# Kernel optimization log

Hardware: AMD Instinct MI355X
Metric: run time of the kernel (lower is better)

## Reference

```python
import jax, jax.numpy as jnp
import numpy as np

MARGIN = 0.5
EPS = 1e-5


def setup_inputs() -> dict:
    key = jax.random.key(0)
    k1, k2 = jax.random.split(key)
    n, d, n_new, n_old = 8192, 256, 4096, 4096
    feature = jax.random.normal(k1, (n, d), dtype=jnp.float32)
    target = jax.random.randint(k2, (n,), 0, 100, dtype=jnp.int64)
    new_idx = jnp.arange(n_new, dtype=jnp.int64)
    old_idx = jnp.arange(n_old, dtype=jnp.int64)
    return {"feature": feature, "target": target, "new_idx": new_idx, "old_idx": old_idx}


def _triplet_loss(feature, target, new_idx, old_idx):
    n = feature.shape[0]
    n_new = new_idx.shape[0]
    # alpha switch is based on static shape, exactly as in the torch code
    alpha = 0.9 if old_idx.shape[0] != 0 else 0.5

    sim = feature @ feature.T                      # [n, n]
    sim_new = sim[:, new_idx]                      # [n, n_new]
    t_new = target[new_idx]                        # [n_new]

    same_new = target[:, None] == t_new[None, :]   # [n, n_new]
    is_new_row = jnp.arange(n) < n_new             # [n]

    # positive pairs (only defined for rows i < n_new)
    pos_mask = same_new & (sim_new < 1.0 - EPS)
    pos_loss_new = jnp.sum(jnp.where(pos_mask, 1.0 - sim_new, 0.0), axis=1)  # [n]
    # faithful to the torch bug: rows i >= n_new reuse the stale pos_pair_
    # from the last new row (i = n_new - 1)
    stale_pos = pos_loss_new[n_new - 1]
    pos_loss = jnp.where(is_new_row, pos_loss_new, stale_pos)

    # negatives: new rows scan all columns, old rows scan only new_idx columns
    diff_all = target[:, None] != target[None, :]
    neg_all = jnp.sum(jnp.where(diff_all & (sim > MARGIN), sim, 0.0), axis=1)
    neg_newcols = jnp.sum(jnp.where((~same_new) & (sim_new > MARGIN), sim_new, 0.0), axis=1)
    neg_loss = jnp.where(is_new_row, neg_all, neg_newcols)

    return jnp.mean(alpha * pos_loss + (1.0 - alpha) * neg_loss)


def reference(feature, target, new_idx, old_idx):
    return _triplet_loss(feature, target, new_idx, old_idx)
```

## Files before the change

### kernel.cpp

```cpp
#include <hip/hip_runtime.h>
#include <hip/hip_bf16.h>
#include <stdint.h>

#define MARGIN   0.5f
#define POS_THR  (1.0f - 1e-5f)

typedef __attribute__((ext_vector_type(8))) short  short8;
typedef __attribute__((ext_vector_type(4))) float  f32x4;

#define BM 128
#define BN 128
#define BK 32
#define NPANEL_SHIFT 7
#define NSLOTS 256
#define MAXN_HIST 8192

__device__ __forceinline__ ushort f2bf_rne(float x) {
  uint32_t u = __float_as_uint(x);
  u += 0x7fffu + ((u >> 16) & 1u);
  return (ushort)(u >> 16);
}

__device__ __forceinline__ void async_load16(const ushort* g, ushort* l) {
  __builtin_amdgcn_global_load_lds(
      (__attribute__((address_space(1))) void*)(const_cast<ushort*>(g)),
      (__attribute__((address_space(3))) void*)(l),
      16, 0, 0);
}

__global__ void prep_kernel(const float* __restrict__ src, ushort* __restrict__ dst,
                            const int* __restrict__ new_idx,
                            int* __restrict__ cnt, int* __restrict__ flags,
                            float* __restrict__ misc,
                            int total8, int n, int npanel, int n_new, int convBlocks) {
  __shared__ int hcnt[MAXN_HIST];
  __shared__ int hflag[MAXN_HIST / BN];
  const int tid = threadIdx.x;
  if ((int)blockIdx.x < convBlocks) {
    int i = blockIdx.x * blockDim.x + tid;
    if (i < total8) {
      const float4* s4 = reinterpret_cast<const float4*>(src);
      float4 a = s4[i * 2], b = s4[i * 2 + 1];
      short8 o;
      o[0] = (short)f2bf_rne(a.x); o[1] = (short)f2bf_rne(a.y);
      o[2] = (short)f2bf_rne(a.z); o[3] = (short)f2bf_rne(a.w);
      o[4] = (short)f2bf_rne(b.x); o[5] = (short)f2bf_rne(b.y);
      o[6] = (short)f2bf_rne(b.z); o[7] = (short)f2bf_rne(b.w);
      reinterpret_cast<short8*>(dst)[i] = o;
    }
    return;
  }
  for (int i = tid; i < n; i += blockDim.x) hcnt[i] = 0;
  for (int i = tid; i < npanel; i += blockDim.x) hflag[i] = 0;
  __syncthreads();
  for (int i = tid; i < n_new; i += blockDim.x) atomicAdd(&hcnt[new_idx[i]], 1);
  __syncthreads();
  for (int i = tid; i < n; i += blockDim.x) {
    int c = hcnt[i];
    cnt[i] = c;
    if (c) atomicOr(&hflag[i >> NPANEL_SHIFT], 1);
  }
  __syncthreads();
  for (int i = tid; i < npanel; i += blockDim.x) flags[i] = hflag[i];
  for (int i = tid; i < NSLOTS + 1; i += blockDim.x) misc[i] = 0.f;
}

__global__ __launch_bounds__(256) void simloss_kernel(
    const ushort* __restrict__ fb, const int* __restrict__ target,
    const int* __restrict__ cnt, const int* __restrict__ flags,
    float* __restrict__ misc, int d, int n_new, float alpha) {
  __shared__ __align__(16) ushort Als[3][BM * BK];
  __shared__ __align__(16) ushort Bls[3][BN * BK];
  __shared__ int   t_row[BM];
  __shared__ int   t_col[BN];
  __shared__ float cw_col[BN];
  __shared__ float cw_row[BM];
  __shared__ float red[4];

  const int bx = blockIdx.x, by = blockIdx.y;
  if (bx > by) return;
  const int tid = threadIdx.x;
  const int rowBase = by * BM;
  const int colBase = bx * BN;
  const bool diag = (bx == by);

  if ((rowBase >= n_new && flags[bx] == 0) &&
      (colBase >= n_new && flags[by] == 0)) return;

  if (tid < BM) {
    t_row[tid]  = target[rowBase + tid];
    cw_row[tid] = (float)cnt[rowBase + tid];
  }
  if (tid < BN) {
    t_col[tid]  = target[colBase + tid];
    cw_col[tid] = (float)cnt[colBase + tid];
  }

  const int lane = tid & 63;
  const int wid  = tid >> 6;
  const int wr   = wid >> 1;
  const int wc   = wid & 1;
  const int l15  = lane & 15;
  const int kb   = lane >> 4;

  const int ch0 = (wid * 2 + 0) * 64 + lane;
  const int ch1 = (wid * 2 + 1) * 64 + lane;
  const int r0 = ch0 >> 2, kq0 = (ch0 & 3) ^ ((ch0 >> 3) & 3);
  const int r1 = ch1 >> 2, kq1 = (ch1 & 3) ^ ((ch1 >> 3) & 3);
  const ushort* gA0 = fb + (size_t)(rowBase + r0) * d + kq0 * 8;
  const ushort* gA1 = fb + (size_t)(rowBase + r1) * d + kq1 * 8;
  const ushort* gB0 = fb + (size_t)(colBase + r0) * d + kq0 * 8;
  const ushort* gB1 = fb + (size_t)(colBase + r1) * d + kq1 * 8;
  const int lo0 = (wid * 2 + 0) * 512;
  const int lo1 = (wid * 2 + 1) * 512;

  f32x4 acc[4][4] = {};

  int aoff[4], boff[4];
#pragma unroll
  for (int m = 0; m < 4; ++m) {
    int row = wr * 64 + m * 16 + l15;
    aoff[m] = row * 32 + ((kb ^ ((row >> 1) & 3)) * 8);
  }
#pragma unroll
  for (int nf = 0; nf < 4; ++nf) {
    int row = wc * 64 + nf * 16 + l15;
    boff[nf] = row * 32 + ((kb ^ ((row >> 1) & 3)) * 8);
  }

  asm volatile("s_waitcnt vmcnt(0) lgkmcnt(0)" ::: "memory");
  __builtin_amdgcn_sched_barrier(0);

  async_load16(gA0, &Als[0][lo0]);
  async_load16(gA1, &Als[0][lo1]);
  async_load16(gB0, &Bls[0][lo0]);
  async_load16(gB1, &Bls[0][lo1]);
  const int nk = d / BK;
  if (nk > 1) {
    async_load16(gA0 + BK, &Als[1][lo0]);
    async_load16(gA1 + BK, &Als[1][lo1]);
    async_load16(gB0 + BK, &Bls[1][lo0]);
    async_load16(gB1 + BK, &Bls[1][lo1]);
  }

  int cur = 0;
  for (int t = 0; t < nk; ++t) {
    if (t == nk - 1) asm volatile("s_waitcnt vmcnt(0)" ::: "memory");
    else             asm volatile("s_waitcnt vmcnt(4)" ::: "memory");
    __builtin_amdgcn_s_barrier();
    __builtin_amdgcn_sched_barrier(0);

    if (t + 2 < nk) {
      int nxt = cur + 2; if (nxt >= 3) nxt -= 3;
      int ko = (t + 2) * BK;
      async_load16(gA0 + ko, &Als[nxt][lo0]);
      async_load16(gA1 + ko, &Als[nxt][lo1]);
      async_load16(gB0 + ko, &Bls[nxt][lo0]);
      async_load16(gB1 + ko, &Bls[nxt][lo1]);
    }

    short8 afr[4], bfr[4];
#pragma unroll
    for (int m = 0; m < 4; ++m)
      afr[m] = *reinterpret_cast<const short8*>(&Als[cur][aoff[m]]);
#pragma unroll
    for (int nf = 0; nf < 4; ++nf)
      bfr[nf] = *reinterpret_cast<const short8*>(&Bls[cur][boff[nf]]);
    asm volatile("s_waitcnt lgkmcnt(0)" ::: "memory");
    __builtin_amdgcn_sched_barrier(0);

#pragma unroll
    for (int m = 0; m < 4; ++m)
#pragma unroll
      for (int nf = 0; nf < 4; ++nf)
        acc[m][nf] = __builtin_amdgcn_mfma_f32_16x16x32_bf16(bfr[nf], afr[m], acc[m][nf], 0, 0, 0);

    cur = (cur + 1 == 3) ? 0 : cur + 1;
  }

  const float beta = 1.0f - alpha;
  int tc_r[4][4]; float cw_c[4][4]; bool cn_r[4][4];
#pragma unroll
  for (int nf = 0; nf < 4; ++nf)
#pragma unroll
    for (int q = 0; q < 4; ++q) {
      int cl = wc * 64 + nf * 16 + kb * 4 + q;
      tc_r[nf][q] = t_col[cl];
      cw_c[nf][q] = cw_col[cl];
      cn_r[nf][q] = (colBase + cl) < n_new;
    }

  const int  stale_row = n_new - 1;
  const bool blk_stale = (stale_row >= rowBase) && (stale_row < rowBase + BM);
  const int  srl = stale_row - rowBase;

  float tot = 0.f;
#pragma unroll
  for (int m = 0; m < 4; ++m) {
    int rl = wr * 64 + m * 16 + l15;
    int r  = rowBase + rl;
    int tr = t_row[rl];
    bool rnew = (r < n_new);
    float cwr  = cw_row[rl];
    float acwr = alpha * cwr;
    float bcwr = beta * cwr;
    float p = 0.f, ng = 0.f, t2 = 0.f;
#pragma unroll
    for (int nf = 0; nf < 4; ++nf)
#pragma unroll
      for (int q = 0; q < 4; ++q) {
        float s = acc[m][nf][q];
        bool same = (tr == tc_r[nf][q]);
        bool gm = (s > MARGIN);
        bool lp = (s < POS_THR);
        if (rnew) {
          if (same && lp) p  += cw_c[nf][q] * (1.0f - s);
          if (!same && gm) ng += s;
        } else {
          if (!same && gm) ng += cw_c[nf][q] * s;
        }
        if (cn_r[nf][q]) {
          if (same && lp)  t2 += acwr * (1.0f - s);
          if (!same && gm) t2 += beta * s;
        } else {
          if (!same && gm) t2 += bcwr * s;
        }
      }
    if (blk_stale && wr == (srl >> 6) && m == ((srl >> 4) & 3)) {
      float pr = p;
      pr += __shfl_xor(pr, 16); pr += __shfl_xor(pr, 32);
      if (lane < 16 && rl == srl) atomicAdd(&misc[NSLOTS], pr);
    }
    tot += rnew ? fmaf(alpha, p, beta * ng) : beta * ng;
    if (!diag) tot += t2;
  }
#pragma unroll
  for (int off = 32; off; off >>= 1) tot += __shfl_xor(tot, off);
  if (lane == 0) red[wid] = tot;
  __syncthreads();
  if (tid == 0)
    atomicAdd(&misc[(by * gridDim.x + bx) & (NSLOTS - 1)],
              red[0] + red[1] + red[2] + red[3]);
}

__global__ void finalize_kernel(const float* __restrict__ misc,
                                float* __restrict__ out, int n, int n_new,
                                float alpha) {
  int t = threadIdx.x;
  float c = misc[t] + misc[t + 64] + misc[t + 128] + misc[t + 192];
#pragma unroll
  for (int off = 32; off; off >>= 1) c += __shfl_xor(c, off);
  if (t == 0)
    out[0] = (c + (float)(n - n_new) * alpha * misc[NSLOTS]) / (float)n;
}

extern "C" void kernel_launch(void* const* d_in, const int* in_sizes, int n_in,
                              void* d_out, int out_size, void* d_ws, size_t ws_size,
                              hipStream_t stream) {
  const float* feature = (const float*)d_in[0];
  const int*   target  = (const int*)d_in[1];
  const int*   new_idx = (const int*)d_in[2];

  const int n     = in_sizes[1];
  const int d     = in_sizes[0] / n;
  const int n_new = in_sizes[2];
  const int n_old = (n_in > 3) ? in_sizes[3] : 0;
  const float alpha = (n_old != 0) ? 0.9f : 0.5f;
  const int npanel = n / BN;

  auto al = [](size_t x) { return (x + 255) & ~(size_t)255; };
  char* ws = (char*)d_ws;
  ushort* fb    = (ushort*)ws;
  size_t  off   = al((size_t)n * d * sizeof(ushort));
  int*    cnt   = (int*)(ws + off);   off += al((size_t)n * sizeof(int));
  int*    flags = (int*)(ws + off);   off += al((size_t)npanel * sizeof(int));
  float*  misc  = (float*)(ws + off);

  int total8 = (n * d) / 8;
  int convBlocks = (total8 + 255) / 256;
  prep_kernel<<<convBlocks + 1, 256, 0, stream>>>(feature, fb, new_idx, cnt, flags,
                                                  misc, total8, n, npanel,
                                                  n_new, convBlocks);

  dim3 grid(n / BN, n / BM);
  simloss_kernel<<<grid, 256, 0, stream>>>(fb, target, cnt, flags, misc,
                                           d, n_new, alpha);

  finalize_kernel<<<1, 64, 0, stream>>>(misc, (float*)d_out, n, n_new, alpha);
}
```

Before: 125.8 us.

## Use persistent blocks over a compacted tile list with cross-tile prefetch

The prep kernel now builds a compacted list of active lower-triangle tiles with a prefix scan, and packs target and count into one int2 metadata array. The similarity kernel becomes persistent: 512 blocks walk the list and prefetch the next tile's first K stages and metadata while the current tile finishes, using a 4-stage buffer. This removes launch and early-exit cost for the many skipped blocks and hides pipeline fill latency between tiles. It also adds a serial list build inside one prep block and fixed hand-tuned vmcnt counts that depend on d/BK being 8.

```diff
diff --git a/kernel.cpp b/kernel.cpp
--- a/kernel.cpp
+++ b/kernel.cpp
@@ -11,9 +11,9 @@
 #define BM 128
 #define BN 128
 #define BK 32
-#define NPANEL_SHIFT 7
 #define NSLOTS 256
 #define MAXN_HIST 8192
+#define NB 512
 
 __device__ __forceinline__ ushort f2bf_rne(float x) {
   uint32_t u = __float_as_uint(x);
@@ -28,13 +28,14 @@
       16, 0, 0);
 }
 
-__global__ void prep_kernel(const float* __restrict__ src, ushort* __restrict__ dst,
-                            const int* __restrict__ new_idx,
-                            int* __restrict__ cnt, int* __restrict__ flags,
-                            float* __restrict__ misc,
-                            int total8, int n, int npanel, int n_new, int convBlocks) {
-  __shared__ int hcnt[MAXN_HIST];
-  __shared__ int hflag[MAXN_HIST / BN];
+#define WAITV(N) asm volatile("s_waitcnt vmcnt(" #N ")" ::: "memory")
+
+__global__ __launch_bounds__(256) void prep_kernel(
+    const float* __restrict__ src, ushort* __restrict__ dst,
+    const int* __restrict__ target, const int* __restrict__ new_idx,
+    int2* __restrict__ metaG, int* __restrict__ list, int* __restrict__ nActG,
+    float* __restrict__ misc, int total8, int n, int npanel, int n_new,
+    int convBlocks) {
   const int tid = threadIdx.x;
   if ((int)blockIdx.x < convBlocks) {
     int i = blockIdx.x * blockDim.x + tid;
@@ -50,71 +51,88 @@
     }
     return;
   }
-  for (int i = tid; i < n; i += blockDim.x) hcnt[i] = 0;
-  for (int i = tid; i < npanel; i += blockDim.x) hflag[i] = 0;
-  __syncthreads();
-  for (int i = tid; i < n_new; i += blockDim.x) atomicAdd(&hcnt[new_idx[i]], 1);
-  __syncthreads();
-  for (int i = tid; i < n; i += blockDim.x) {
+  __shared__ int hcnt[MAXN_HIST];
+  __shared__ int hflag[MAXN_HIST / BN];
+  __shared__ int pcnt[256];
+  for (int i = tid; i < n; i += 256) hcnt[i] = 0;
+  for (int i = tid; i < npanel; i += 256) hflag[i] = 0;
+  __syncthreads();
+  for (int i = tid; i < n_new; i += 256) atomicAdd(&hcnt[new_idx[i]], 1);
+  __syncthreads();
+  for (int i = tid; i < n; i += 256) {
     int c = hcnt[i];
-    cnt[i] = c;
-    if (c) atomicOr(&hflag[i >> NPANEL_SHIFT], 1);
-  }
-  __syncthreads();
-  for (int i = tid; i < npanel; i += blockDim.x) flags[i] = hflag[i];
-  for (int i = tid; i < NSLOTS + 1; i += blockDim.x) misc[i] = 0.f;
-}
-
-__global__ __launch_bounds__(256) void simloss_kernel(
-    const ushort* __restrict__ fb, const int* __restrict__ target,
-    const int* __restrict__ cnt, const int* __restrict__ flags,
+    metaG[i] = make_int2(target[i], __float_as_int((float)c));
+    if (c) atomicOr(&hflag[i >> 7], 1);
+  }
+  for (int i = tid; i < NSLOTS + 1; i += 256) misc[i] = 0.f;
+  __syncthreads();
+  const int P  = npanel;
+  const int TP = P * (P + 1) / 2;
+  const int C  = (TP + 255) / 256;
+  int l0 = tid * C, l1 = min(l0 + C, TP);
+  int cnt_t = 0;
+  int by = 0, bx = 0;
+  if (l0 < TP) {
+    by = (int)((sqrtf(8.f * (float)l0 + 1.f) - 1.f) * 0.5f);
+    while ((by + 1) * (by + 2) / 2 <= l0) by++;
+    while (by * (by + 1) / 2 > l0) by--;
+    bx = l0 - by * (by + 1) / 2;
+    int tby = by, tbx = bx;
+    for (int l = l0; l < l1; ++l) {
+      bool rowOld = tby * BM >= n_new, colOld = tbx * BN >= n_new;
+      if (!((rowOld && hflag[tbx] == 0) && (colOld && hflag[tby] == 0))) cnt_t++;
+      if (++tbx > tby) { tby++; tbx = 0; }
+    }
+  }
+  pcnt[tid] = cnt_t;
+  __syncthreads();
+  for (int off = 1; off < 256; off <<= 1) {
+    int v = (tid >= off) ? pcnt[tid - off] : 0;
+    __syncthreads();
+    pcnt[tid] += v;
+    __syncthreads();
+  }
+  int pos = pcnt[tid] - cnt_t;
+  if (tid == 255) *nActG = pcnt[255];
+  if (l0 < TP) {
+    for (int l = l0; l < l1; ++l) {
+      bool rowOld = by * BM >= n_new, colOld = bx * BN >= n_new;
+      if (!((rowOld && hflag[bx] == 0) && (colOld && hflag[by] == 0)))
+        list[pos++] = (by << 16) | bx;
+      if (++bx > by) { by++; bx = 0; }
+    }
+  }
+}
+
+__global__ __launch_bounds__(256, 2) void simloss_kernel(
+    const ushort* __restrict__ fb, const int2* __restrict__ metaG,
+    const int* __restrict__ list, const int* __restrict__ nActG,
     float* __restrict__ misc, int d, int n_new, float alpha) {
-  __shared__ __align__(16) ushort Als[3][BM * BK];
-  __shared__ __align__(16) ushort Bls[3][BN * BK];
-  __shared__ int   t_row[BM];
-  __shared__ int   t_col[BN];
-  __shared__ float cw_col[BN];
-  __shared__ float cw_row[BM];
+  __shared__ __align__(16) ushort Als[4][BM * BK];
+  __shared__ __align__(16) ushort Bls[4][BN * BK];
+  __shared__ __align__(16) int2  metaRl[2][BM];
+  __shared__ __align__(16) int2  metaCl[2][BN];
   __shared__ float red[4];
 
-  const int bx = blockIdx.x, by = blockIdx.y;
-  if (bx > by) return;
-  const int tid = threadIdx.x;
-  const int rowBase = by * BM;
-  const int colBase = bx * BN;
-  const bool diag = (bx == by);
-
-  if ((rowBase >= n_new && flags[bx] == 0) &&
-      (colBase >= n_new && flags[by] == 0)) return;
-
-  if (tid < BM) {
-    t_row[tid]  = target[rowBase + tid];
-    cw_row[tid] = (float)cnt[rowBase + tid];
-  }
-  if (tid < BN) {
-    t_col[tid]  = target[colBase + tid];
-    cw_col[tid] = (float)cnt[colBase + tid];
-  }
-
+  const int bid  = blockIdx.x;
+  const int nAct = *nActG;
+  if (bid >= nAct) return;
+
+  const int tid  = threadIdx.x;
   const int lane = tid & 63;
   const int wid  = tid >> 6;
   const int wr   = wid >> 1;
   const int wc   = wid & 1;
   const int l15  = lane & 15;
   const int kb   = lane >> 4;
+  const float beta = 1.0f - alpha;
 
   const int ch0 = (wid * 2 + 0) * 64 + lane;
   const int ch1 = (wid * 2 + 1) * 64 + lane;
   const int r0 = ch0 >> 2, kq0 = (ch0 & 3) ^ ((ch0 >> 3) & 3);
   const int r1 = ch1 >> 2, kq1 = (ch1 & 3) ^ ((ch1 >> 3) & 3);
-  const ushort* gA0 = fb + (size_t)(rowBase + r0) * d + kq0 * 8;
-  const ushort* gA1 = fb + (size_t)(rowBase + r1) * d + kq1 * 8;
-  const ushort* gB0 = fb + (size_t)(colBase + r0) * d + kq0 * 8;
-  const ushort* gB1 = fb + (size_t)(colBase + r1) * d + kq1 * 8;
   const int lo0 = (wid * 2 + 0) * 512;
   const int lo1 = (wid * 2 + 1) * 512;
-
-  f32x4 acc[4][4] = {};
 
   int aoff[4], boff[4];
 #pragma unroll
@@ -128,119 +146,156 @@
     boff[nf] = row * 32 + ((kb ^ ((row >> 1) & 3)) * 8);
   }
 
+  int w  = bid;
+  int pk = list[w];
+  int curRow = (pk >> 16) * BM, curCol = (pk & 0xffff) * BN;
+  const ushort* cA0 = fb + (size_t)(curRow + r0) * d + kq0 * 8;
+  const ushort* cA1 = fb + (size_t)(curRow + r1) * d + kq1 * 8;
+  const ushort* cB0 = fb + (size_t)(curCol + r0) * d + kq0 * 8;
+  const ushort* cB1 = fb + (size_t)(curCol + r1) * d + kq1 * 8;
+  const ushort* cMR = (const ushort*)(metaG + curRow) + (size_t)lane * 8;
+  const ushort* cMC = (const ushort*)(metaG + curCol) + (size_t)lane * 8;
+
+  f32x4 acc[4][4] = {};
+  float tot = 0.f;
+  int mp = 0;
+
   asm volatile("s_waitcnt vmcnt(0) lgkmcnt(0)" ::: "memory");
   __builtin_amdgcn_sched_barrier(0);
-
-  async_load16(gA0, &Als[0][lo0]);
-  async_load16(gA1, &Als[0][lo1]);
-  async_load16(gB0, &Bls[0][lo0]);
-  async_load16(gB1, &Bls[0][lo1]);
-  const int nk = d / BK;
-  if (nk > 1) {
-    async_load16(gA0 + BK, &Als[1][lo0]);
-    async_load16(gA1 + BK, &Als[1][lo1]);
-    async_load16(gB0 + BK, &Bls[1][lo0]);
-    async_load16(gB1 + BK, &Bls[1][lo1]);
-  }
-
-  int cur = 0;
-  for (int t = 0; t < nk; ++t) {
-    if (t == nk - 1) asm volatile("s_waitcnt vmcnt(0)" ::: "memory");
-    else             asm volatile("s_waitcnt vmcnt(4)" ::: "memory");
-    __builtin_amdgcn_s_barrier();
-    __builtin_amdgcn_sched_barrier(0);
-
-    if (t + 2 < nk) {
-      int nxt = cur + 2; if (nxt >= 3) nxt -= 3;
-      int ko = (t + 2) * BK;
-      async_load16(gA0 + ko, &Als[nxt][lo0]);
-      async_load16(gA1 + ko, &Als[nxt][lo1]);
-      async_load16(gB0 + ko, &Bls[nxt][lo0]);
-      async_load16(gB1 + ko, &Bls[nxt][lo1]);
-    }
-
-    short8 afr[4], bfr[4];
-#pragma unroll
-    for (int m = 0; m < 4; ++m)
-      afr[m] = *reinterpret_cast<const short8*>(&Als[cur][aoff[m]]);
-#pragma unroll
-    for (int nf = 0; nf < 4; ++nf)
-      bfr[nf] = *reinterpret_cast<const short8*>(&Bls[cur][boff[nf]]);
-    asm volatile("s_waitcnt lgkmcnt(0)" ::: "memory");
-    __builtin_amdgcn_sched_barrier(0);
-
-#pragma unroll
-    for (int m = 0; m < 4; ++m)
-#pragma unroll
-      for (int nf = 0; nf < 4; ++nf)
-        acc[m][nf] = __builtin_amdgcn_mfma_f32_16x16x32_bf16(bfr[nf], afr[m], acc[m][nf], 0, 0, 0);
-
-    cur = (cur + 1 == 3) ? 0 : cur + 1;
-  }
-
-  const float beta = 1.0f - alpha;
-  int tc_r[4][4]; float cw_c[4][4]; bool cn_r[4][4];
-#pragma unroll
-  for (int nf = 0; nf < 4; ++nf)
-#pragma unroll
-    for (int q = 0; q < 4; ++q) {
-      int cl = wc * 64 + nf * 16 + kb * 4 + q;
-      tc_r[nf][q] = t_col[cl];
-      cw_c[nf][q] = cw_col[cl];
-      cn_r[nf][q] = (colBase + cl) < n_new;
-    }
-
-  const int  stale_row = n_new - 1;
-  const bool blk_stale = (stale_row >= rowBase) && (stale_row < rowBase + BM);
-  const int  srl = stale_row - rowBase;
-
-  float tot = 0.f;
-#pragma unroll
-  for (int m = 0; m < 4; ++m) {
-    int rl = wr * 64 + m * 16 + l15;
-    int r  = rowBase + rl;
-    int tr = t_row[rl];
-    bool rnew = (r < n_new);
-    float cwr  = cw_row[rl];
-    float acwr = alpha * cwr;
-    float bcwr = beta * cwr;
-    float p = 0.f, ng = 0.f, t2 = 0.f;
-#pragma unroll
-    for (int nf = 0; nf < 4; ++nf)
-#pragma unroll
-      for (int q = 0; q < 4; ++q) {
-        float s = acc[m][nf][q];
-        bool same = (tr == tc_r[nf][q]);
-        bool gm = (s > MARGIN);
-        bool lp = (s < POS_THR);
-        if (rnew) {
-          if (same && lp) p  += cw_c[nf][q] * (1.0f - s);
-          if (!same && gm) ng += s;
+#define STAGE4(pa0, pa1, pb0, pb1, p)                                          \
+  { async_load16((pa0) + (p) * BK, &Als[(p) & 3][lo0]);                        \
+    async_load16((pa1) + (p) * BK, &Als[(p) & 3][lo1]);                        \
+    async_load16((pb0) + (p) * BK, &Bls[(p) & 3][lo0]);                        \
+    async_load16((pb1) + (p) * BK, &Bls[(p) & 3][lo1]); }
+  STAGE4(cA0, cA1, cB0, cB1, 0);
+  async_load16(cMR, (ushort*)&metaRl[0][0]);
+  async_load16(cMC, (ushort*)&metaCl[0][0]);
+  STAGE4(cA0, cA1, cB0, cB1, 1);
+  STAGE4(cA0, cA1, cB0, cB1, 2);
+
+  for (;;) {
+    const bool hasNext = (w + NB) < nAct;
+    const int  pkN = hasNext ? list[w + NB] : pk;
+    const int  nxtRow = (pkN >> 16) * BM, nxtCol = (pkN & 0xffff) * BN;
+    const ushort* nA0 = fb + (size_t)(nxtRow + r0) * d + kq0 * 8;
+    const ushort* nA1 = fb + (size_t)(nxtRow + r1) * d + kq1 * 8;
+    const ushort* nB0 = fb + (size_t)(nxtCol + r0) * d + kq0 * 8;
+    const ushort* nB1 = fb + (size_t)(nxtCol + r1) * d + kq1 * 8;
+    const ushort* nMR = (const ushort*)(metaG + nxtRow) + (size_t)lane * 8;
+    const ushort* nMC = (const ushort*)(metaG + nxtCol) + (size_t)lane * 8;
+
+#pragma unroll
+    for (int i = 0; i < 8; ++i) {
+      if (i < 6)        WAITV(8);
+      else if (i == 6)  { if (hasNext) WAITV(10); else WAITV(4); }
+      else              { if (hasNext) WAITV(10); else WAITV(0); }
+      __builtin_amdgcn_s_barrier();
+      __builtin_amdgcn_sched_barrier(0);
+
+      if (i <= 4) {
+        STAGE4(cA0, cA1, cB0, cB1, i + 3);
+      } else if (hasNext) {
+        if (i == 5) {
+          STAGE4(nA0, nA1, nB0, nB1, 0);
+          async_load16(nMR, (ushort*)&metaRl[mp ^ 1][0]);
+          async_load16(nMC, (ushort*)&metaCl[mp ^ 1][0]);
+        } else if (i == 6) {
+          STAGE4(nA0, nA1, nB0, nB1, 1);
         } else {
-          if (!same && gm) ng += cw_c[nf][q] * s;
-        }
-        if (cn_r[nf][q]) {
-          if (same && lp)  t2 += acwr * (1.0f - s);
-          if (!same && gm) t2 += beta * s;
-        } else {
-          if (!same && gm) t2 += bcwr * s;
+          STAGE4(nA0, nA1, nB0, nB1, 2);
         }
       }
-    if (blk_stale && wr == (srl >> 6) && m == ((srl >> 4) & 3)) {
-      float pr = p;
-      pr += __shfl_xor(pr, 16); pr += __shfl_xor(pr, 32);
-      if (lane < 16 && rl == srl) atomicAdd(&misc[NSLOTS], pr);
-    }
-    tot += rnew ? fmaf(alpha, p, beta * ng) : beta * ng;
-    if (!diag) tot += t2;
-  }
+
+      short8 afr[4], bfr[4];
+      const ushort* As = &Als[i & 3][0];
+      const ushort* Bs = &Bls[i & 3][0];
+#pragma unroll
+      for (int m = 0; m < 4; ++m)
+        afr[m] = *reinterpret_cast<const short8*>(&As[aoff[m]]);
+#pragma unroll
+      for (int nf = 0; nf < 4; ++nf)
+        bfr[nf] = *reinterpret_cast<const short8*>(&Bs[boff[nf]]);
+      asm volatile("s_waitcnt lgkmcnt(0)" ::: "memory");
+      __builtin_amdgcn_sched_barrier(0);
+
+#pragma unroll
+      for (int m = 0; m < 4; ++m)
+#pragma unroll
+        for (int nf = 0; nf < 4; ++nf)
+          acc[m][nf] = __builtin_amdgcn_mfma_f32_16x16x32_bf16(bfr[nf], afr[m], acc[m][nf], 0, 0, 0);
+    }
+
+    {
+      const bool diag = (curRow == curCol);
+      int tcr[4][4]; float cwc[4][4]; bool cnr[4][4];
+#pragma unroll
+      for (int nf = 0; nf < 4; ++nf)
+#pragma unroll
+        for (int q = 0; q < 4; ++q) {
+          int cl = wc * 64 + nf * 16 + kb * 4 + q;
+          int2 mc = metaCl[mp][cl];
+          tcr[nf][q] = mc.x;
+          cwc[nf][q] = __int_as_float(mc.y);
+          cnr[nf][q] = (curCol + cl) < n_new;
+        }
+      const int  stale_row = n_new - 1;
+      const bool blk_stale = (stale_row >= curRow) && (stale_row < curRow + BM);
+      const int  srl = stale_row - curRow;
+#pragma unroll
+      for (int m = 0; m < 4; ++m) {
+        int rl = wr * 64 + m * 16 + l15;
+        int r  = curRow + rl;
+        int2 mr = metaRl[mp][rl];
+        int   tr  = mr.x;
+        float cwr = __int_as_float(mr.y);
+        bool rnew = (r < n_new);
+        float acwr = alpha * cwr, bcwr = beta * cwr;
+        float p = 0.f, ng = 0.f, t2 = 0.f;
+#pragma unroll
+        for (int nf = 0; nf < 4; ++nf)
+#pragma unroll
+          for (int q = 0; q < 4; ++q) {
+            float s = acc[m][nf][q];
+            bool same = (tr == tcr[nf][q]);
+            bool gm = (s > MARGIN);
+            bool lp = (s < POS_THR);
+            if (rnew) {
+              if (same && lp)  p  += cwc[nf][q] * (1.0f - s);
+              if (!same && gm) ng += s;
+            } else {
+              if (!same && gm) ng += cwc[nf][q] * s;
+            }
+            if (cnr[nf][q]) {
+              if (same && lp)  t2 += acwr * (1.0f - s);
+              if (!same && gm) t2 += beta * s;
+            } else {
+              if (!same && gm) t2 += bcwr * s;
+            }
+          }
+        if (blk_stale && wr == (srl >> 6) && m == ((srl >> 4) & 3)) {
+          float pr = p;
+          pr += __shfl_xor(pr, 16); pr += __shfl_xor(pr, 32);
+          if (lane < 16 && rl == srl) atomicAdd(&misc[NSLOTS], pr);
+        }
+        tot += rnew ? fmaf(alpha, p, beta * ng) : beta * ng;
+        if (!diag) tot += t2;
+        acc[m][0] = f32x4{}; acc[m][1] = f32x4{};
+        acc[m][2] = f32x4{}; acc[m][3] = f32x4{};
+      }
+    }
+
+    if (!hasNext) break;
+    w += NB; pk = pkN; mp ^= 1;
+    curRow = nxtRow; curCol = nxtCol;
+    cA0 = nA0; cA1 = nA1; cB0 = nB0; cB1 = nB1;
+  }
+
 #pragma unroll
   for (int off = 32; off; off >>= 1) tot += __shfl_xor(tot, off);
   if (lane == 0) red[wid] = tot;
   __syncthreads();
   if (tid == 0)
-    atomicAdd(&misc[(by * gridDim.x + bx) & (NSLOTS - 1)],
-              red[0] + red[1] + red[2] + red[3]);
+    atomicAdd(&misc[bid & (NSLOTS - 1)], red[0] + red[1] + red[2] + red[3]);
 }
 
 __global__ void finalize_kernel(const float* __restrict__ misc,
@@ -267,24 +322,26 @@
   const int n_old = (n_in > 3) ? in_sizes[3] : 0;
   const float alpha = (n_old != 0) ? 0.9f : 0.5f;
   const int npanel = n / BN;
+  const int maxTiles = npanel * (npanel + 1) / 2;
 
   auto al = [](size_t x) { return (x + 255) & ~(size_t)255; };
   char* ws = (char*)d_ws;
   ushort* fb    = (ushort*)ws;
   size_t  off   = al((size_t)n * d * sizeof(ushort));
-  int*    cnt   = (int*)(ws + off);   off += al((size_t)n * sizeof(int));
-  int*    flags = (int*)(ws + off);   off += al((size_t)npanel * sizeof(int));
+  int2*   metaG = (int2*)(ws + off);  off += al((size_t)n * sizeof(int2));
+  int*    list  = (int*)(ws + off);   off += al((size_t)maxTiles * sizeof(int));
+  int*    nAct  = (int*)(ws + off);   off += al(sizeof(int));
   float*  misc  = (float*)(ws + off);
 
   int total8 = (n * d) / 8;
   int convBlocks = (total8 + 255) / 256;
-  prep_kernel<<<convBlocks + 1, 256, 0, stream>>>(feature, fb, new_idx, cnt, flags,
-                                                  misc, total8, n, npanel,
-                                                  n_new, convBlocks);
-
-  dim3 grid(n / BN, n / BM);
-  simloss_kernel<<<grid, 256, 0, stream>>>(fb, target, cnt, flags, misc,
-                                           d, n_new, alpha);
+  prep_kernel<<<convBlocks + 1, 256, 0, stream>>>(feature, fb, target, new_idx,
+                                                  metaG, list, nAct, misc,
+                                                  total8, n, npanel, n_new,
+                                                  convBlocks);
+
+  simloss_kernel<<<NB, 256, 0, stream>>>(fb, metaG, list, nAct, misc,
+                                         d, n_new, alpha);
 
   finalize_kernel<<<1, 64, 0, stream>>>(misc, (float*)d_out, n, n_new, alpha);
 }
```

After: 123.4 us. No clear change (-1.9%).

## Load MFMA fragments directly from global memory and launch only lower-triangle tiles

Applied to the files above, without the earlier changes.

Drops the LDS triple-buffered async-load pipeline and has each wave read its bf16 MFMA fragments straight from global memory, relying on L2/L1 reuse. It launches a 1D grid over only the lower-triangular tiles, recovering (bx,by) with a sqrt-based index decode, instead of a square grid where half the blocks exit at once. It also packs target and count into one int2 metadata array built in the prep kernel, so each tile needs fewer metadata loads. The risk is that uncoalesced per-lane 16-byte global loads, with no staging through shared memory, cost more than the LDS pipeline and the removed early-exit blocks saved.

```diff
diff --git a/kernel.cpp b/kernel.cpp
--- a/kernel.cpp
+++ b/kernel.cpp
@@ -10,8 +10,6 @@
 
 #define BM 128
 #define BN 128
-#define BK 32
-#define NPANEL_SHIFT 7
 #define NSLOTS 256
 #define MAXN_HIST 8192
 
@@ -21,20 +19,11 @@
   return (ushort)(u >> 16);
 }
 
-__device__ __forceinline__ void async_load16(const ushort* g, ushort* l) {
-  __builtin_amdgcn_global_load_lds(
-      (__attribute__((address_space(1))) void*)(const_cast<ushort*>(g)),
-      (__attribute__((address_space(3))) void*)(l),
-      16, 0, 0);
-}
-
-__global__ void prep_kernel(const float* __restrict__ src, ushort* __restrict__ dst,
-                            const int* __restrict__ new_idx,
-                            int* __restrict__ cnt, int* __restrict__ flags,
-                            float* __restrict__ misc,
-                            int total8, int n, int npanel, int n_new, int convBlocks) {
-  __shared__ int hcnt[MAXN_HIST];
-  __shared__ int hflag[MAXN_HIST / BN];
+__global__ __launch_bounds__(256) void prep_kernel(
+    const float* __restrict__ src, ushort* __restrict__ dst,
+    const int* __restrict__ target, const int* __restrict__ new_idx,
+    int2* __restrict__ metaG, int* __restrict__ flags, float* __restrict__ misc,
+    int total8, int n, int npanel, int n_new, int convBlocks) {
   const int tid = threadIdx.x;
   if ((int)blockIdx.x < convBlocks) {
     int i = blockIdx.x * blockDim.x + tid;
@@ -50,52 +39,43 @@
     }
     return;
   }
-  for (int i = tid; i < n; i += blockDim.x) hcnt[i] = 0;
-  for (int i = tid; i < npanel; i += blockDim.x) hflag[i] = 0;
-  __syncthreads();
-  for (int i = tid; i < n_new; i += blockDim.x) atomicAdd(&hcnt[new_idx[i]], 1);
-  __syncthreads();
-  for (int i = tid; i < n; i += blockDim.x) {
+  __shared__ int hcnt[MAXN_HIST];
+  __shared__ int hflag[MAXN_HIST / BN];
+  for (int i = tid; i < n; i += 256) hcnt[i] = 0;
+  for (int i = tid; i < npanel; i += 256) hflag[i] = 0;
+  __syncthreads();
+  for (int i = tid; i < n_new; i += 256) atomicAdd(&hcnt[new_idx[i]], 1);
+  __syncthreads();
+  for (int i = tid; i < n; i += 256) {
     int c = hcnt[i];
-    cnt[i] = c;
-    if (c) atomicOr(&hflag[i >> NPANEL_SHIFT], 1);
-  }
-  __syncthreads();
-  for (int i = tid; i < npanel; i += blockDim.x) flags[i] = hflag[i];
-  for (int i = tid; i < NSLOTS + 1; i += blockDim.x) misc[i] = 0.f;
+    metaG[i] = make_int2(target[i], __float_as_int((float)c));
+    if (c) atomicOr(&hflag[i >> 7], 1);
+  }
+  __syncthreads();
+  for (int i = tid; i < npanel; i += 256) flags[i] = hflag[i];
+  for (int i = tid; i < NSLOTS + 1; i += 256) misc[i] = 0.f;
 }
 
 __global__ __launch_bounds__(256) void simloss_kernel(
-    const ushort* __restrict__ fb, const int* __restrict__ target,
-    const int* __restrict__ cnt, const int* __restrict__ flags,
-    float* __restrict__ misc, int d, int n_new, float alpha) {
-  __shared__ __align__(16) ushort Als[3][BM * BK];
-  __shared__ __align__(16) ushort Bls[3][BN * BK];
-  __shared__ int   t_row[BM];
-  __shared__ int   t_col[BN];
-  __shared__ float cw_col[BN];
-  __shared__ float cw_row[BM];
+    const ushort* __restrict__ fb, const int2* __restrict__ metaG,
+    const int* __restrict__ flags, float* __restrict__ misc,
+    int d, int n_new, float alpha) {
+  __shared__ int2 metaR[BM];
+  __shared__ int2 metaC[BN];
   __shared__ float red[4];
 
-  const int bx = blockIdx.x, by = blockIdx.y;
-  if (bx > by) return;
-  const int tid = threadIdx.x;
+  const int l = blockIdx.x;
+  int by = (int)((sqrtf(8.f * (float)l + 1.f) - 1.f) * 0.5f);
+  while ((by + 1) * (by + 2) / 2 <= l) by++;
+  while (by * (by + 1) / 2 > l) by--;
+  const int bx = l - by * (by + 1) / 2;
+
   const int rowBase = by * BM;
   const int colBase = bx * BN;
-  const bool diag = (bx == by);
-
   if ((rowBase >= n_new && flags[bx] == 0) &&
       (colBase >= n_new && flags[by] == 0)) return;
 
-  if (tid < BM) {
-    t_row[tid]  = target[rowBase + tid];
-    cw_row[tid] = (float)cnt[rowBase + tid];
-  }
-  if (tid < BN) {
-    t_col[tid]  = target[colBase + tid];
-    cw_col[tid] = (float)cnt[colBase + tid];
-  }
-
+  const int tid  = threadIdx.x;
   const int lane = tid & 63;
   const int wid  = tid >> 6;
   const int wr   = wid >> 1;
@@ -103,91 +83,43 @@
   const int l15  = lane & 15;
   const int kb   = lane >> 4;
 
-  const int ch0 = (wid * 2 + 0) * 64 + lane;
-  const int ch1 = (wid * 2 + 1) * 64 + lane;
-  const int r0 = ch0 >> 2, kq0 = (ch0 & 3) ^ ((ch0 >> 3) & 3);
-  const int r1 = ch1 >> 2, kq1 = (ch1 & 3) ^ ((ch1 >> 3) & 3);
-  const ushort* gA0 = fb + (size_t)(rowBase + r0) * d + kq0 * 8;
-  const ushort* gA1 = fb + (size_t)(rowBase + r1) * d + kq1 * 8;
-  const ushort* gB0 = fb + (size_t)(colBase + r0) * d + kq0 * 8;
-  const ushort* gB1 = fb + (size_t)(colBase + r1) * d + kq1 * 8;
-  const int lo0 = (wid * 2 + 0) * 512;
-  const int lo1 = (wid * 2 + 1) * 512;
+  if (tid < BM)        metaR[tid]       = metaG[rowBase + tid];
+  else if (tid < 256)  metaC[tid - 128] = metaG[colBase + (tid - 128)];
+  __syncthreads();
+
+  const ushort* pA = fb + (size_t)(rowBase + wr * 64 + l15) * d + kb * 8;
+  const ushort* pB = fb + (size_t)(colBase + wc * 64 + l15) * d + kb * 8;
 
   f32x4 acc[4][4] = {};
-
-  int aoff[4], boff[4];
-#pragma unroll
-  for (int m = 0; m < 4; ++m) {
-    int row = wr * 64 + m * 16 + l15;
-    aoff[m] = row * 32 + ((kb ^ ((row >> 1) & 3)) * 8);
-  }
-#pragma unroll
-  for (int nf = 0; nf < 4; ++nf) {
-    int row = wc * 64 + nf * 16 + l15;
-    boff[nf] = row * 32 + ((kb ^ ((row >> 1) & 3)) * 8);
-  }
-
-  asm volatile("s_waitcnt vmcnt(0) lgkmcnt(0)" ::: "memory");
-  __builtin_amdgcn_sched_barrier(0);
-
-  async_load16(gA0, &Als[0][lo0]);
-  async_load16(gA1, &Als[0][lo1]);
-  async_load16(gB0, &Bls[0][lo0]);
-  async_load16(gB1, &Bls[0][lo1]);
-  const int nk = d / BK;
-  if (nk > 1) {
-    async_load16(gA0 + BK, &Als[1][lo0]);
-    async_load16(gA1 + BK, &Als[1][lo1]);
-    async_load16(gB0 + BK, &Bls[1][lo0]);
-    async_load16(gB1 + BK, &Bls[1][lo1]);
-  }
-
-  int cur = 0;
-  for (int t = 0; t < nk; ++t) {
-    if (t == nk - 1) asm volatile("s_waitcnt vmcnt(0)" ::: "memory");
-    else             asm volatile("s_waitcnt vmcnt(4)" ::: "memory");
-    __builtin_amdgcn_s_barrier();
-    __builtin_amdgcn_sched_barrier(0);
-
-    if (t + 2 < nk) {
-      int nxt = cur + 2; if (nxt >= 3) nxt -= 3;
-      int ko = (t + 2) * BK;
-      async_load16(gA0 + ko, &Als[nxt][lo0]);
-      async_load16(gA1 + ko, &Als[nxt][lo1]);
-      async_load16(gB0 + ko, &Bls[nxt][lo0]);
-      async_load16(gB1 + ko, &Bls[nxt][lo1]);
-    }
-
+  const int nk = d >> 5;
+#pragma unroll 2
+  for (int ks = 0; ks < nk; ++ks) {
     short8 afr[4], bfr[4];
 #pragma unroll
     for (int m = 0; m < 4; ++m)
-      afr[m] = *reinterpret_cast<const short8*>(&Als[cur][aoff[m]]);
+      afr[m] = *reinterpret_cast<const short8*>(pA + (size_t)m * 16 * d + ks * 32);
 #pragma unroll
     for (int nf = 0; nf < 4; ++nf)
-      bfr[nf] = *reinterpret_cast<const short8*>(&Bls[cur][boff[nf]]);
-    asm volatile("s_waitcnt lgkmcnt(0)" ::: "memory");
-    __builtin_amdgcn_sched_barrier(0);
-
+      bfr[nf] = *reinterpret_cast<const short8*>(pB + (size_t)nf * 16 * d + ks * 32);
 #pragma unroll
     for (int m = 0; m < 4; ++m)
 #pragma unroll
       for (int nf = 0; nf < 4; ++nf)
         acc[m][nf] = __builtin_amdgcn_mfma_f32_16x16x32_bf16(bfr[nf], afr[m], acc[m][nf], 0, 0, 0);
-
-    cur = (cur + 1 == 3) ? 0 : cur + 1;
   }
 
   const float beta = 1.0f - alpha;
-  int tc_r[4][4]; float cw_c[4][4]; bool cn_r[4][4];
+  const bool diag = (bx == by);
+  int tcr[4][4]; float cwc[4][4]; bool cnr[4][4];
 #pragma unroll
   for (int nf = 0; nf < 4; ++nf)
 #pragma unroll
     for (int q = 0; q < 4; ++q) {
       int cl = wc * 64 + nf * 16 + kb * 4 + q;
-      tc_r[nf][q] = t_col[cl];
-      cw_c[nf][q] = cw_col[cl];
-      cn_r[nf][q] = (colBase + cl) < n_new;
+      int2 mc = metaC[cl];
+      tcr[nf][q] = mc.x;
+      cwc[nf][q] = __int_as_float(mc.y);
+      cnr[nf][q] = (colBase + cl) < n_new;
     }
 
   const int  stale_row = n_new - 1;
@@ -199,27 +131,27 @@
   for (int m = 0; m < 4; ++m) {
     int rl = wr * 64 + m * 16 + l15;
     int r  = rowBase + rl;
-    int tr = t_row[rl];
+    int2 mr = metaR[rl];
+    int   tr  = mr.x;
+    float cwr = __int_as_float(mr.y);
     bool rnew = (r < n_new);
-    float cwr  = cw_row[rl];
-    float acwr = alpha * cwr;
-    float bcwr = beta * cwr;
+    float acwr = alpha * cwr, bcwr = beta * cwr;
     float p = 0.f, ng = 0.f, t2 = 0.f;
 #pragma unroll
     for (int nf = 0; nf < 4; ++nf)
 #pragma unroll
       for (int q = 0; q < 4; ++q) {
         float s = acc[m][nf][q];
-        bool same = (tr == tc_r[nf][q]);
+        bool same = (tr == tcr[nf][q]);
         bool gm = (s > MARGIN);
         bool lp = (s < POS_THR);
         if (rnew) {
-          if (same && lp) p  += cw_c[nf][q] * (1.0f - s);
+          if (same && lp)  p  += cwc[nf][q] * (1.0f - s);
           if (!same && gm) ng += s;
         } else {
-          if (!same && gm) ng += cw_c[nf][q] * s;
+          if (!same && gm) ng += cwc[nf][q] * s;
         }
-        if (cn_r[nf][q]) {
+        if (cnr[nf][q]) {
           if (same && lp)  t2 += acwr * (1.0f - s);
           if (!same && gm) t2 += beta * s;
         } else {
@@ -239,8 +171,7 @@
   if (lane == 0) red[wid] = tot;
   __syncthreads();
   if (tid == 0)
-    atomicAdd(&misc[(by * gridDim.x + bx) & (NSLOTS - 1)],
-              red[0] + red[1] + red[2] + red[3]);
+    atomicAdd(&misc[blockIdx.x & (NSLOTS - 1)], red[0] + red[1] + red[2] + red[3]);
 }
 
 __global__ void finalize_kernel(const float* __restrict__ misc,
@@ -267,24 +198,25 @@
   const int n_old = (n_in > 3) ? in_sizes[3] : 0;
   const float alpha = (n_old != 0) ? 0.9f : 0.5f;
   const int npanel = n / BN;
+  const int nTiles = npanel * (npanel + 1) / 2;
 
   auto al = [](size_t x) { return (x + 255) & ~(size_t)255; };
   char* ws = (char*)d_ws;
   ushort* fb    = (ushort*)ws;
   size_t  off   = al((size_t)n * d * sizeof(ushort));
-  int*    cnt   = (int*)(ws + off);   off += al((size_t)n * sizeof(int));
+  int2*   metaG = (int2*)(ws + off);  off += al((size_t)n * sizeof(int2));
   int*    flags = (int*)(ws + off);   off += al((size_t)npanel * sizeof(int));
   float*  misc  = (float*)(ws + off);
 
   int total8 = (n * d) / 8;
   int convBlocks = (total8 + 255) / 256;
-  prep_kernel<<<convBlocks + 1, 256, 0, stream>>>(feature, fb, new_idx, cnt, flags,
-                                                  misc, total8, n, npanel,
-                                                  n_new, convBlocks);
-
-  dim3 grid(n / BN, n / BM);
-  simloss_kernel<<<grid, 256, 0, stream>>>(fb, target, cnt, flags, misc,
-                                           d, n_new, alpha);
+  prep_kernel<<<convBlocks + 1, 256, 0, stream>>>(feature, fb, target, new_idx,
+                                                  metaG, flags, misc,
+                                                  total8, n, npanel, n_new,
+                                                  convBlocks);
+
+  simloss_kernel<<<nTiles, 256, 0, stream>>>(fb, metaG, flags, misc,
+                                             d, n_new, alpha);
 
   finalize_kernel<<<1, 64, 0, stream>>>(misc, (float*)d_out, n, n_new, alpha);
 }
```

New measurement: 150.1 us. 1.19x slower.
